# Optimization experiments

Hardware: AMD Instinct MI355X
Metric: run time of the kernel (lower is better)

## Reference

```python
import jax, jax.numpy as jnp
import numpy as np

B, S, D = 32, 1, 2048
H, KVH, HD = 16, 4, 128
MAXS = 4096
EPS = 1e-5
NREP = H // KVH  # GQA repeat factor = 4
FF = 4 * D
POS = 4095  # decode position (start_pos)


def setup_inputs() -> dict:
    key = jax.random.key(0)
    ks = jax.random.split(key, 12)
    sc = lambda d: 1.0 / np.sqrt(d)
    # RoPE angles for the current token position, [S, HD//2]
    inv_freq = 1.0 / (10000.0 ** (np.arange(0, HD, 2, dtype=np.float32) / HD))
    ang = (POS + np.arange(S, dtype=np.float32))[:, None] * inv_freq[None, :]
    return {
        "x": jax.random.normal(ks[0], (B, S, D), jnp.float32),
        "cos": jnp.asarray(np.cos(ang), jnp.float32),
        "sin": jnp.asarray(np.sin(ang), jnp.float32),
        "k_cache": jax.random.normal(ks[1], (B, MAXS, KVH, HD), jnp.float32),
        "v_cache": jax.random.normal(ks[2], (B, MAXS, KVH, HD), jnp.float32),
        "w_rms_attn": jnp.ones((D,), jnp.float32),
        "wq": jax.random.normal(ks[3], (D, D), jnp.float32) * sc(D),
        "wk": jax.random.normal(ks[4], (D, KVH * HD), jnp.float32) * sc(D),
        "wv": jax.random.normal(ks[5], (D, KVH * HD), jnp.float32) * sc(D),
        "wo": jax.random.normal(ks[6], (D, D), jnp.float32) * sc(D),
        "w_rms_ffn": jnp.ones((D,), jnp.float32),
        "w1": jax.random.normal(ks[7], (D, FF), jnp.float32) * sc(D),
        "w2": jax.random.normal(ks[8], (D, FF), jnp.float32) * sc(D),
        "w3": jax.random.normal(ks[9], (FF, D), jnp.float32) * sc(FF),
        "start_pos": POS,
    }


def _rmsnorm(x, g):
    return x * g * jax.lax.rsqrt(jnp.mean(x * x, axis=-1, keepdims=True) + EPS)


def _rope(x, cos, sin):
    # x: [B, S, h, HD]; complex rotation on (even, odd) pairs
    xr = x.reshape(*x.shape[:-1], HD // 2, 2)
    x0, x1 = xr[..., 0], xr[..., 1]
    c = cos[None, :, None, :]
    s = sin[None, :, None, :]
    r0 = x0 * c - x1 * s
    r1 = x0 * s + x1 * c
    return jnp.stack([r0, r1], axis=-1).reshape(x.shape)


def reference(x, cos, sin, k_cache, v_cache, w_rms_attn, wq, wk, wv, wo,
              w_rms_ffn, w1, w2, w3, start_pos):
    xa = _rmsnorm(x, w_rms_attn)
    xq = (xa @ wq).reshape(B, S, H, HD)
    xk = (xa @ wk).reshape(B, S, KVH, HD)
    xv = (xa @ wv).reshape(B, S, KVH, HD)
    # Source applies RoPE to K and V (not Q) -- reproduced faithfully.
    xk = _rope(xk, cos, sin)
    xv = _rope(xv, cos, sin)
    kc = jax.lax.dynamic_update_slice(k_cache, xk, (0, start_pos, 0, 0))
    vc = jax.lax.dynamic_update_slice(v_cache, xv, (0, start_pos, 0, 0))
    klen = start_pos + S
    keys = jnp.repeat(kc[:, :klen], NREP, axis=2)   # [B, klen, H, HD]
    vals = jnp.repeat(vc[:, :klen], NREP, axis=2)
    att = jnp.einsum('bqhd,bkhd->bhqk', xq, keys) * (HD ** -0.5)
    att = jax.nn.softmax(att, axis=-1)
    y = jnp.einsum('bhqk,bkhd->bqhd', att, vals).reshape(B, S, D)
    h = x + y @ wo
    xf = _rmsnorm(h, w_rms_ffn)
    return h + (jax.nn.silu(xf @ w1) * (xf @ w2)) @ w3
```

## Files before the change

### kernel.cpp

```cpp
#include <hip/hip_runtime.h>
#include <math.h>

#define BB 32
#define DD 2048
#define NKVH 4
#define HDIM 128
#define MAXS 4096
#define FFD 8192
#define POS 4095
#define EPSV 1e-5f
#define SCALE 0.08838834764831845f
#define ASPLIT 16

#define OFF_QT   0u
#define OFF_KT   65536u
#define OFF_VT   81920u
#define OFF_G1   98304u
#define OFF_G2   360448u
#define ZERO_N   622592u
#define OFF_XAT  622592u
#define OFF_RK   688128u
#define OFF_RV   704512u
#define OFF_PML  720896u
#define OFF_PACC 737280u
#define OFF_YT   1785856u
#define OFF_H    1851392u
#define OFF_XFT  1916928u

#define REP32(M) M(0) M(1) M(2) M(3) M(4) M(5) M(6) M(7) M(8) M(9) M(10) M(11) M(12) M(13) M(14) M(15) M(16) M(17) M(18) M(19) M(20) M(21) M(22) M(23) M(24) M(25) M(26) M(27) M(28) M(29) M(30) M(31)
#define REP32A(M,X) M(0,X) M(1,X) M(2,X) M(3,X) M(4,X) M(5,X) M(6,X) M(7,X) M(8,X) M(9,X) M(10,X) M(11,X) M(12,X) M(13,X) M(14,X) M(15,X) M(16,X) M(17,X) M(18,X) M(19,X) M(20,X) M(21,X) M(22,X) M(23,X) M(24,X) M(25,X) M(26,X) M(27,X) M(28,X) M(29,X) M(30,X) M(31,X)

#define DECLA(i) float a##i = 0.f;
#define FMA1(i,k) a##i = fmaf(ap[(k)*32 + (i)], w##k, a##i);
#define STORET(i) tl[i] = a##i;
#define ATOMN(i) atomicAdd(C + (size_t)(i)*N + n, a##i);

template<int N, int CH, bool TOUT>
__device__ __forceinline__ void gemv_body(const float* __restrict__ At,
                                          const float* __restrict__ W,
                                          float* __restrict__ C, int colblk,
                                          float* tile) {
    int tid = (int)threadIdx.x;
    int n = colblk * 256 + tid;
    int d0 = blockIdx.y * CH;
    const float* Wp = W + (size_t)d0 * N + n;
    const float* ap = At + (size_t)d0 * 32;
    REP32(DECLA)
#pragma unroll 4
    for (int dd = 0; dd < CH; dd += 4) {
        float w0 = Wp[0];
        float w1 = Wp[(size_t)N];
        float w2 = Wp[(size_t)N * 2];
        float w3 = Wp[(size_t)N * 3];
        REP32A(FMA1, 0)
        REP32A(FMA1, 1)
        REP32A(FMA1, 2)
        REP32A(FMA1, 3)
        Wp += (size_t)N * 4;
        ap += 128;
    }
    if constexpr (TOUT) {
        float* tl = tile + tid * 33;
        REP32(STORET)
        __syncthreads();
        float* cb = C + (size_t)colblk * 256 * 32;
#pragma unroll
        for (int i = 0; i < 32; ++i) {
            int f = i * 256 + tid;
            atomicAdd(cb + f, tile[(f >> 5) * 33 + (f & 31)]);
        }
    } else {
        REP32(ATOMN)
    }
}

template<int N, int CH, bool TOUT>
__global__ __launch_bounds__(256) void gemv32_kernel(const float* __restrict__ At,
                                                     const float* __restrict__ W,
                                                     float* __restrict__ C) {
    if constexpr (TOUT) {
        __shared__ float tile[256 * 33];
        gemv_body<N, CH, true>(At, W, C, blockIdx.x, tile);
    } else {
        gemv_body<N, CH, false>(At, W, C, blockIdx.x, nullptr);
    }
}

template<int N, int CH, int HALF>
__global__ __launch_bounds__(256) void gemv32_dual_kernel(const float* __restrict__ At,
        const float* __restrict__ W0, const float* __restrict__ W1,
        float* __restrict__ C0, float* __restrict__ C1) {
    __shared__ float tile[256 * 33];
    int bx = blockIdx.x;
    if (bx < HALF) gemv_body<N, CH, true>(At, W0, C0, bx, tile);
    else           gemv_body<N, CH, true>(At, W1, C1, bx - HALF, tile);
}

__global__ void zero_kernel(float* __restrict__ p) {
    p[blockIdx.x * 256 + threadIdx.x] = 0.f;
}

__global__ void rmsnorm_kernel(const float* __restrict__ in, const float* __restrict__ g,
                               float* __restrict__ outT, float* __restrict__ cpy) {
    int b = blockIdx.x;
    int tid = threadIdx.x;
    const float* row = in + b * DD;
    float v[8];
    float ss = 0.f;
#pragma unroll
    for (int i = 0; i < 8; ++i) { v[i] = row[tid + i * 256]; ss += v[i] * v[i]; }
#pragma unroll
    for (int off = 32; off; off >>= 1) ss += __shfl_xor(ss, off);
    __shared__ float red[4];
    if ((tid & 63) == 0) red[tid >> 6] = ss;
    __syncthreads();
    ss = red[0] + red[1] + red[2] + red[3];
    float scale = rsqrtf(ss * (1.f / DD) + EPSV);
#pragma unroll
    for (int i = 0; i < 8; ++i) {
        int idx = tid + i * 256;
        outT[(size_t)idx * 32 + b] = v[i] * g[idx] * scale;
        if (cpy) cpy[b * DD + idx] = v[i];
    }
}

__global__ void rope_kernel(const float* __restrict__ kT, const float* __restrict__ vT,
                            const float* __restrict__ cosb, const float* __restrict__ sinb,
                            float* __restrict__ rk, float* __restrict__ rv) {
    int idx = blockIdx.x * 256 + threadIdx.x;
    int b = idx >> 8, rem = idx & 255;
    int kvh = rem >> 6, i = rem & 63;
    float c = cosb[i], s = sinb[i];
    int col = kvh * HDIM + 2 * i;
    float k0 = kT[(size_t)col * 32 + b], k1 = kT[(size_t)(col + 1) * 32 + b];
    float v0 = vT[(size_t)col * 32 + b], v1 = vT[(size_t)(col + 1) * 32 + b];
    int o = (b * NKVH + kvh) * HDIM + 2 * i;
    rk[o] = k0 * c - k1 * s; rk[o + 1] = k0 * s + k1 * c;
    rv[o] = v0 * c - v1 * s; rv[o + 1] = v0 * s + v1 * c;
}

__global__ __launch_bounds__(256) void attn_partial_kernel(
    const float* __restrict__ qT, const float* __restrict__ kc, const float* __restrict__ vc,
    const float* __restrict__ rk, const float* __restrict__ rv,
    float* __restrict__ pml, float* __restrict__ pacc) {
    int bid = blockIdx.x;
    int split = bid & 15, kvh = (bid >> 4) & 3, b = bid >> 6;
    int tid = threadIdx.x;
    __shared__ float q_s[4][HDIM];
    __shared__ float p_s[4][256];
    __shared__ float red[8][4][HDIM];
    for (int i = tid; i < 4 * HDIM; i += 256)
        q_s[i >> 7][i & 127] = qT[(size_t)(kvh * 512 + i) * 32 + b];
    __syncthreads();
    int t0 = split * 256;
    {
        int t = t0 + tid;
        const float* krow = (t == POS) ? rk + (b * NKVH + kvh) * HDIM
                                       : kc + ((size_t)(b * MAXS + t) * NKVH + kvh) * HDIM;
        float s0 = 0, s1 = 0, s2 = 0, s3 = 0;
#pragma unroll 8
        for (int j = 0; j < HDIM; j += 4) {
            float4 kk = *(const float4*)(krow + j);
            s0 += kk.x * q_s[0][j] + kk.y * q_s[0][j + 1] + kk.z * q_s[0][j + 2] + kk.w * q_s[0][j + 3];
            s1 += kk.x * q_s[1][j] + kk.y * q_s[1][j + 1] + kk.z * q_s[1][j + 2] + kk.w * q_s[1][j + 3];
            s2 += kk.x * q_s[2][j] + kk.y * q_s[2][j + 1] + kk.z * q_s[2][j + 2] + kk.w * q_s[2][j + 3];
            s3 += kk.x * q_s[3][j] + kk.y * q_s[3][j + 1] + kk.z * q_s[3][j + 2] + kk.w * q_s[3][j + 3];
        }
        p_s[0][tid] = s0 * SCALE; p_s[1][tid] = s1 * SCALE;
        p_s[2][tid] = s2 * SCALE; p_s[3][tid] = s3 * SCALE;
    }
    __syncthreads();
    {
        int w = tid >> 6, lane = tid & 63;
        float e0 = p_s[w][lane], e1 = p_s[w][lane + 64];
        float e2 = p_s[w][lane + 128], e3 = p_s[w][lane + 192];
        float m = fmaxf(fmaxf(e0, e1), fmaxf(e2, e3));
#pragma unroll
        for (int off = 32; off; off >>= 1) m = fmaxf(m, __shfl_xor(m, off));
        e0 = __expf(e0 - m); e1 = __expf(e1 - m);
        e2 = __expf(e2 - m); e3 = __expf(e3 - m);
        p_s[w][lane] = e0; p_s[w][lane + 64] = e1;
        p_s[w][lane + 128] = e2; p_s[w][lane + 192] = e3;
        float l = e0 + e1 + e2 + e3;
#pragma unroll
        for (int off = 32; off; off >>= 1) l += __shfl_xor(l, off);
        if (lane == 0) {
            int idx = ((b * NKVH + kvh) * ASPLIT + split) * 4 + w;
            pml[2 * idx] = m; pml[2 * idx + 1] = l;
        }
    }
    __syncthreads();
    {
        int tsub = tid >> 5, q4 = tid & 31;
        int tb = t0 + tsub * 32;
        const float* vbase = vc + ((size_t)(b * MAXS + tb) * NKVH + kvh) * HDIM + q4 * 4;
        float4 a0 = {0, 0, 0, 0}, a1 = a0, a2 = a0, a3 = a0;
        int jmax = (split == ASPLIT - 1 && tsub == 7) ? 31 : 32;
#pragma unroll 4
        for (int j = 0; j < jmax; ++j) {
            float4 vv = *(const float4*)(vbase + (size_t)j * (NKVH * HDIM));
            int tl = tsub * 32 + j;
            float p0 = p_s[0][tl], p1 = p_s[1][tl], p2 = p_s[2][tl], p3 = p_s[3][tl];
            a0.x = fmaf(p0, vv.x, a0.x); a0.y = fmaf(p0, vv.y, a0.y); a0.z = fmaf(p0, vv.z, a0.z); a0.w = fmaf(p0, vv.w, a0.w);
            a1.x = fmaf(p1, vv.x, a1.x); a1.y = fmaf(p1, vv.y, a1.y); a1.z = fmaf(p1, vv.z, a1.z); a1.w = fmaf(p1, vv.w, a1.w);
            a2.x = fmaf(p2, vv.x, a2.x); a2.y = fmaf(p2, vv.y, a2.y); a2.z = fmaf(p2, vv.z, a2.z); a2.w = fmaf(p2, vv.w, a2.w);
            a3.x = fmaf(p3, vv.x, a3.x); a3.y = fmaf(p3, vv.y, a3.y); a3.z = fmaf(p3, vv.z, a3.z); a3.w = fmaf(p3, vv.w, a3.w);
        }
        if (split == ASPLIT - 1 && tsub == 7) {
            float4 vv = *(const float4*)(rv + (b * NKVH + kvh) * HDIM + q4 * 4);
            float p0 = p_s[0][255], p1 = p_s[1][255], p2 = p_s[2][255], p3 = p_s[3][255];
            a0.x = fmaf(p0, vv.x, a0.x); a0.y = fmaf(p0, vv.y, a0.y); a0.z = fmaf(p0, vv.z, a0.z); a0.w = fmaf(p0, vv.w, a0.w);
            a1.x = fmaf(p1, vv.x, a1.x); a1.y = fmaf(p1, vv.y, a1.y); a1.z = fmaf(p1, vv.z, a1.z); a1.w = fmaf(p1, vv.w, a1.w);
            a2.x = fmaf(p2, vv.x, a2.x); a2.y = fmaf(p2, vv.y, a2.y); a2.z = fmaf(p2, vv.z, a2.z); a2.w = fmaf(p2, vv.w, a2.w);
            a3.x = fmaf(p3, vv.x, a3.x); a3.y = fmaf(p3, vv.y, a3.y); a3.z = fmaf(p3, vv.z, a3.z); a3.w = fmaf(p3, vv.w, a3.w);
        }
        *(float4*)&red[tsub][0][q4 * 4] = a0;
        *(float4*)&red[tsub][1][q4 * 4] = a1;
        *(float4*)&red[tsub][2][q4 * 4] = a2;
        *(float4*)&red[tsub][3][q4 * 4] = a3;
    }
    __syncthreads();
    if (tid < 128) {
        int h = tid >> 5, qq = tid & 31;
        float4 s = {0, 0, 0, 0};
#pragma unroll
        for (int r = 0; r < 8; ++r) {
            float4 t4 = *(const float4*)&red[r][h][qq * 4];
            s.x += t4.x; s.y += t4.y; s.z += t4.z; s.w += t4.w;
        }
        int idx = ((b * NKVH + kvh) * ASPLIT + split) * 4 + h;
        *(float4*)(pacc + (size_t)idx * HDIM + qq * 4) = s;
    }
}

__global__ void attn_combine_kernel(const float* __restrict__ pml,
                                    const float* __restrict__ pacc, float* __restrict__ yT) {
    int bid = blockIdx.x;
    int b = bid >> 4, h = bid & 15;
    int kvh = h >> 2, hl = h & 3;
    int d = threadIdx.x;
    float M = -INFINITY;
#pragma unroll
    for (int s = 0; s < ASPLIT; ++s) {
        int idx = ((b * NKVH + kvh) * ASPLIT + s) * 4 + hl;
        M = fmaxf(M, pml[2 * idx]);
    }
    float denom = 0.f, acc = 0.f;
#pragma unroll
    for (int s = 0; s < ASPLIT; ++s) {
        int idx = ((b * NKVH + kvh) * ASPLIT + s) * 4 + hl;
        float e = __expf(pml[2 * idx] - M);
        denom += pml[2 * idx + 1] * e;
        acc += e * pacc[(size_t)idx * HDIM + d];
    }
    yT[(size_t)(h * HDIM + d) * 32 + b] = acc / denom;
}

__global__ void silu_mul_kernel(float* __restrict__ g1, const float* __restrict__ g2) {
    int i = blockIdx.x * 256 + threadIdx.x;
    float a = g1[i], bb = g2[i];
    g1[i] = a * bb / (1.f + __expf(-a));
}

extern "C" void kernel_launch(void* const* d_in, const int* in_sizes, int n_in,
                              void* d_out, int out_size, void* d_ws, size_t ws_size,
                              hipStream_t stream) {
    (void)in_sizes; (void)n_in; (void)out_size; (void)ws_size;
    const float* x    = (const float*)d_in[0];
    const float* cosb = (const float*)d_in[1];
    const float* sinb = (const float*)d_in[2];
    const float* kc   = (const float*)d_in[3];
    const float* vc   = (const float*)d_in[4];
    const float* wra  = (const float*)d_in[5];
    const float* wq   = (const float*)d_in[6];
    const float* wk   = (const float*)d_in[7];
    const float* wv   = (const float*)d_in[8];
    const float* wo   = (const float*)d_in[9];
    const float* wrf  = (const float*)d_in[10];
    const float* w1   = (const float*)d_in[11];
    const float* w2   = (const float*)d_in[12];
    const float* w3   = (const float*)d_in[13];
    float* out = (float*)d_out;
    float* ws  = (float*)d_ws;

    float* qT   = ws + OFF_QT;
    float* kT   = ws + OFF_KT;
    float* vT   = ws + OFF_VT;
    float* g1T  = ws + OFF_G1;
    float* g2T  = ws + OFF_G2;
    float* xaT  = ws + OFF_XAT;
    float* rk   = ws + OFF_RK;
    float* rv   = ws + OFF_RV;
    float* pml  = ws + OFF_PML;
    float* pacc = ws + OFF_PACC;
    float* yT   = ws + OFF_YT;
    float* h    = ws + OFF_H;
    float* xfT  = ws + OFF_XFT;

    zero_kernel<<<ZERO_N / 256, 256, 0, stream>>>(ws);

    rmsnorm_kernel<<<32, 256, 0, stream>>>(x, wra, xaT, h);
    gemv32_kernel<2048, 32, true><<<dim3(8, 64), 256, 0, stream>>>(xaT, wq, qT);
    gemv32_dual_kernel<512, 32, 2><<<dim3(4, 64), 256, 0, stream>>>(xaT, wk, wv, kT, vT);
    rope_kernel<<<32, 256, 0, stream>>>(kT, vT, cosb, sinb, rk, rv);
    attn_partial_kernel<<<2048, 256, 0, stream>>>(qT, kc, vc, rk, rv, pml, pacc);
    attn_combine_kernel<<<512, 128, 0, stream>>>(pml, pacc, yT);
    gemv32_kernel<2048, 32, false><<<dim3(8, 64), 256, 0, stream>>>(yT, wo, h);
    rmsnorm_kernel<<<32, 256, 0, stream>>>(h, wrf, xfT, out);
    gemv32_dual_kernel<8192, 128, 32><<<dim3(64, 16), 256, 0, stream>>>(xfT, w1, w2, g1T, g2T);
    silu_mul_kernel<<<1024, 256, 0, stream>>>(g1T, g2T);
    gemv32_kernel<2048, 128, false><<<dim3(8, 64), 256, 0, stream>>>(g1T, w3, out);
}
```

Baseline: 296.7 us.

## Pipeline attention loads, deepen GEMV unroll and chunking, fold RoPE into a fix buffer

The attention kernel's QK and PV loops are replaced by manually double-buffered register loads (two banks of eight float4 loads), so memory latency on the KV cache overlaps with the FMAs. The GEMV body now loads eight weight rows per iteration, and the Q/O/W3 GEMVs use larger per-block reduction chunks with fewer blocks, which halves the number of atomic partial sums. Q is written directly in row-major form instead of through the transposed shared-tile path. The RoPE kernel becomes a fix-up kernel that writes a 16-position tail copy of K/V, with the current token rotated; only one of those positions is actually read. The rework adds register pressure and some redundant copying in exchange for fewer atomics and better load overlap.

```diff
diff --git a/kernel.cpp b/kernel.cpp
--- a/kernel.cpp
+++ b/kernel.cpp
@@ -11,6 +11,7 @@
 #define EPSV 1e-5f
 #define SCALE 0.08838834764831845f
 #define ASPLIT 16
+#define SPOS 256
 
 #define OFF_QT   0u
 #define OFF_KT   65536u
@@ -19,13 +20,13 @@
 #define OFF_G2   360448u
 #define ZERO_N   622592u
 #define OFF_XAT  622592u
-#define OFF_RK   688128u
-#define OFF_RV   704512u
 #define OFF_PML  720896u
 #define OFF_PACC 737280u
 #define OFF_YT   1785856u
 #define OFF_H    1851392u
 #define OFF_XFT  1916928u
+#define OFF_KFIX 1982464u
+#define OFF_VFIX 2244608u
 
 #define REP32(M) M(0) M(1) M(2) M(3) M(4) M(5) M(6) M(7) M(8) M(9) M(10) M(11) M(12) M(13) M(14) M(15) M(16) M(17) M(18) M(19) M(20) M(21) M(22) M(23) M(24) M(25) M(26) M(27) M(28) M(29) M(30) M(31)
 #define REP32A(M,X) M(0,X) M(1,X) M(2,X) M(3,X) M(4,X) M(5,X) M(6,X) M(7,X) M(8,X) M(9,X) M(10,X) M(11,X) M(12,X) M(13,X) M(14,X) M(15,X) M(16,X) M(17,X) M(18,X) M(19,X) M(20,X) M(21,X) M(22,X) M(23,X) M(24,X) M(25,X) M(26,X) M(27,X) M(28,X) M(29,X) M(30,X) M(31,X)
@@ -34,6 +35,7 @@
 #define FMA1(i,k) a##i = fmaf(ap[(k)*32 + (i)], w##k, a##i);
 #define STORET(i) tl[i] = a##i;
 #define ATOMN(i) atomicAdd(C + (size_t)(i)*N + n, a##i);
+#define LDW(k) float w##k = Wp[(size_t)N * (k)];
 
 template<int N, int CH, bool TOUT>
 __device__ __forceinline__ void gemv_body(const float* __restrict__ At,
@@ -46,18 +48,19 @@
     const float* Wp = W + (size_t)d0 * N + n;
     const float* ap = At + (size_t)d0 * 32;
     REP32(DECLA)
-#pragma unroll 4
-    for (int dd = 0; dd < CH; dd += 4) {
-        float w0 = Wp[0];
-        float w1 = Wp[(size_t)N];
-        float w2 = Wp[(size_t)N * 2];
-        float w3 = Wp[(size_t)N * 3];
+#pragma unroll 2
+    for (int dd = 0; dd < CH; dd += 8) {
+        LDW(0) LDW(1) LDW(2) LDW(3) LDW(4) LDW(5) LDW(6) LDW(7)
         REP32A(FMA1, 0)
         REP32A(FMA1, 1)
         REP32A(FMA1, 2)
         REP32A(FMA1, 3)
-        Wp += (size_t)N * 4;
-        ap += 128;
+        REP32A(FMA1, 4)
+        REP32A(FMA1, 5)
+        REP32A(FMA1, 6)
+        REP32A(FMA1, 7)
+        Wp += (size_t)N * 8;
+        ap += 256;
     }
     if constexpr (TOUT) {
         float* tl = tile + tid * 33;
@@ -124,48 +127,104 @@
     }
 }
 
-__global__ void rope_kernel(const float* __restrict__ kT, const float* __restrict__ vT,
-                            const float* __restrict__ cosb, const float* __restrict__ sinb,
-                            float* __restrict__ rk, float* __restrict__ rv) {
+__global__ void fixrope_kernel(const float* __restrict__ kc, const float* __restrict__ vc,
+                               const float* __restrict__ kT, const float* __restrict__ vT,
+                               const float* __restrict__ cosb, const float* __restrict__ sinb,
+                               float* __restrict__ kfix, float* __restrict__ vfix) {
     int idx = blockIdx.x * 256 + threadIdx.x;
-    int b = idx >> 8, rem = idx & 255;
-    int kvh = rem >> 6, i = rem & 63;
-    float c = cosb[i], s = sinb[i];
-    int col = kvh * HDIM + 2 * i;
-    float k0 = kT[(size_t)col * 32 + b], k1 = kT[(size_t)(col + 1) * 32 + b];
-    float v0 = vT[(size_t)col * 32 + b], v1 = vT[(size_t)(col + 1) * 32 + b];
-    int o = (b * NKVH + kvh) * HDIM + 2 * i;
-    rk[o] = k0 * c - k1 * s; rk[o + 1] = k0 * s + k1 * c;
-    rv[o] = v0 * c - v1 * s; rv[o + 1] = v0 * s + v1 * c;
-}
-
-__global__ __launch_bounds__(256) void attn_partial_kernel(
-    const float* __restrict__ qT, const float* __restrict__ kc, const float* __restrict__ vc,
-    const float* __restrict__ rk, const float* __restrict__ rv,
+    int b = idx >> 13, rem = idx & 8191;
+    int pos = rem >> 9, col = rem & 511;
+    int gpos = 4080 + pos;
+    float kv, vv;
+    if (gpos == POS) {
+        int d = col & 127, i = d >> 1;
+        float c = cosb[i], s = sinb[i];
+        int colp = col & ~1;
+        float k0 = kT[(size_t)colp * 32 + b], k1 = kT[(size_t)(colp + 1) * 32 + b];
+        float v0 = vT[(size_t)colp * 32 + b], v1 = vT[(size_t)(colp + 1) * 32 + b];
+        if (d & 1) { kv = k0 * s + k1 * c; vv = v0 * s + v1 * c; }
+        else       { kv = k0 * c - k1 * s; vv = v0 * c - v1 * s; }
+    } else {
+        size_t o = ((size_t)(b * MAXS + gpos)) * 512 + col;
+        kv = kc[o]; vv = vc[o];
+    }
+    kfix[idx] = kv; vfix[idx] = vv;
+}
+
+
+#define QKSTEP(KK,D0) \
+    s0 = fmaf(KK.x, q_s[0][D0], s0); s0 = fmaf(KK.y, q_s[0][(D0)+1], s0); \
+    s0 = fmaf(KK.z, q_s[0][(D0)+2], s0); s0 = fmaf(KK.w, q_s[0][(D0)+3], s0); \
+    s1 = fmaf(KK.x, q_s[1][D0], s1); s1 = fmaf(KK.y, q_s[1][(D0)+1], s1); \
+    s1 = fmaf(KK.z, q_s[1][(D0)+2], s1); s1 = fmaf(KK.w, q_s[1][(D0)+3], s1); \
+    s2 = fmaf(KK.x, q_s[2][D0], s2); s2 = fmaf(KK.y, q_s[2][(D0)+1], s2); \
+    s2 = fmaf(KK.z, q_s[2][(D0)+2], s2); s2 = fmaf(KK.w, q_s[2][(D0)+3], s2); \
+    s3 = fmaf(KK.x, q_s[3][D0], s3); s3 = fmaf(KK.y, q_s[3][(D0)+1], s3); \
+    s3 = fmaf(KK.z, q_s[3][(D0)+2], s3); s3 = fmaf(KK.w, q_s[3][(D0)+3], s3);
+
+#define QKLOAD(S,JB) \
+    S##0 = *(const float4*)(krow + (JB)*32 + 0);  S##1 = *(const float4*)(krow + (JB)*32 + 4); \
+    S##2 = *(const float4*)(krow + (JB)*32 + 8);  S##3 = *(const float4*)(krow + (JB)*32 + 12); \
+    S##4 = *(const float4*)(krow + (JB)*32 + 16); S##5 = *(const float4*)(krow + (JB)*32 + 20); \
+    S##6 = *(const float4*)(krow + (JB)*32 + 24); S##7 = *(const float4*)(krow + (JB)*32 + 28);
+
+#define QKFMA(S,JB) \
+    QKSTEP(S##0,(JB)*32+0)  QKSTEP(S##1,(JB)*32+4)  QKSTEP(S##2,(JB)*32+8)  QKSTEP(S##3,(JB)*32+12) \
+    QKSTEP(S##4,(JB)*32+16) QKSTEP(S##5,(JB)*32+20) QKSTEP(S##6,(JB)*32+24) QKSTEP(S##7,(JB)*32+28)
+
+#define PVSTEP(VV,P0,P1,P2,P3) \
+    a0.x = fmaf(P0, VV.x, a0.x); a0.y = fmaf(P0, VV.y, a0.y); a0.z = fmaf(P0, VV.z, a0.z); a0.w = fmaf(P0, VV.w, a0.w); \
+    a1.x = fmaf(P1, VV.x, a1.x); a1.y = fmaf(P1, VV.y, a1.y); a1.z = fmaf(P1, VV.z, a1.z); a1.w = fmaf(P1, VV.w, a1.w); \
+    a2.x = fmaf(P2, VV.x, a2.x); a2.y = fmaf(P2, VV.y, a2.y); a2.z = fmaf(P2, VV.z, a2.z); a2.w = fmaf(P2, VV.w, a2.w); \
+    a3.x = fmaf(P3, VV.x, a3.x); a3.y = fmaf(P3, VV.y, a3.y); a3.z = fmaf(P3, VV.z, a3.z); a3.w = fmaf(P3, VV.w, a3.w);
+
+#define PVLOAD(S,JB) \
+    S##0 = *(const float4*)(vbase + (size_t)((JB)*8+0)*512); S##1 = *(const float4*)(vbase + (size_t)((JB)*8+1)*512); \
+    S##2 = *(const float4*)(vbase + (size_t)((JB)*8+2)*512); S##3 = *(const float4*)(vbase + (size_t)((JB)*8+3)*512); \
+    S##4 = *(const float4*)(vbase + (size_t)((JB)*8+4)*512); S##5 = *(const float4*)(vbase + (size_t)((JB)*8+5)*512); \
+    S##6 = *(const float4*)(vbase + (size_t)((JB)*8+6)*512); S##7 = *(const float4*)(vbase + (size_t)((JB)*8+7)*512);
+
+#define PVFMA(S,JB) { \
+    int tl = tsub * 32 + (JB) * 8; \
+    float4 pa0 = *(const float4*)&p_s[0][tl], pb0 = *(const float4*)&p_s[0][tl + 4]; \
+    float4 pa1 = *(const float4*)&p_s[1][tl], pb1 = *(const float4*)&p_s[1][tl + 4]; \
+    float4 pa2 = *(const float4*)&p_s[2][tl], pb2 = *(const float4*)&p_s[2][tl + 4]; \
+    float4 pa3 = *(const float4*)&p_s[3][tl], pb3 = *(const float4*)&p_s[3][tl + 4]; \
+    PVSTEP(S##0, pa0.x, pa1.x, pa2.x, pa3.x) \
+    PVSTEP(S##1, pa0.y, pa1.y, pa2.y, pa3.y) \
+    PVSTEP(S##2, pa0.z, pa1.z, pa2.z, pa3.z) \
+    PVSTEP(S##3, pa0.w, pa1.w, pa2.w, pa3.w) \
+    PVSTEP(S##4, pb0.x, pb1.x, pb2.x, pb3.x) \
+    PVSTEP(S##5, pb0.y, pb1.y, pb2.y, pb3.y) \
+    PVSTEP(S##6, pb0.z, pb1.z, pb2.z, pb3.z) \
+    PVSTEP(S##7, pb0.w, pb1.w, pb2.w, pb3.w) }
+
+__global__ __launch_bounds__(256) void attn_mlp_kernel(
+    const float* __restrict__ qn, const float* __restrict__ kc, const float* __restrict__ vc,
+    const float* __restrict__ kfix, const float* __restrict__ vfix,
     float* __restrict__ pml, float* __restrict__ pacc) {
     int bid = blockIdx.x;
     int split = bid & 15, kvh = (bid >> 4) & 3, b = bid >> 6;
     int tid = threadIdx.x;
     __shared__ float q_s[4][HDIM];
-    __shared__ float p_s[4][256];
+    __shared__ float p_s[4][SPOS];
     __shared__ float red[8][4][HDIM];
-    for (int i = tid; i < 4 * HDIM; i += 256)
-        q_s[i >> 7][i & 127] = qT[(size_t)(kvh * 512 + i) * 32 + b];
-    __syncthreads();
-    int t0 = split * 256;
+    for (int i = tid; i < 512; i += 256)
+        q_s[i >> 7][i & 127] = qn[(size_t)b * DD + kvh * 512 + i];
+    __syncthreads();
+    int t0 = split * SPOS;
     {
         int t = t0 + tid;
-        const float* krow = (t == POS) ? rk + (b * NKVH + kvh) * HDIM
-                                       : kc + ((size_t)(b * MAXS + t) * NKVH + kvh) * HDIM;
-        float s0 = 0, s1 = 0, s2 = 0, s3 = 0;
-#pragma unroll 8
-        for (int j = 0; j < HDIM; j += 4) {
-            float4 kk = *(const float4*)(krow + j);
-            s0 += kk.x * q_s[0][j] + kk.y * q_s[0][j + 1] + kk.z * q_s[0][j + 2] + kk.w * q_s[0][j + 3];
-            s1 += kk.x * q_s[1][j] + kk.y * q_s[1][j + 1] + kk.z * q_s[1][j + 2] + kk.w * q_s[1][j + 3];
-            s2 += kk.x * q_s[2][j] + kk.y * q_s[2][j + 1] + kk.z * q_s[2][j + 2] + kk.w * q_s[2][j + 3];
-            s3 += kk.x * q_s[3][j] + kk.y * q_s[3][j + 1] + kk.z * q_s[3][j + 2] + kk.w * q_s[3][j + 3];
-        }
+        const float* krow = (t == POS)
+            ? kfix + (size_t)b * 8192 + 15 * 512 + kvh * HDIM
+            : kc + ((size_t)(b * MAXS + t) * NKVH + kvh) * HDIM;
+        float s0 = 0.f, s1 = 0.f, s2 = 0.f, s3 = 0.f;
+        float4 A0, A1, A2, A3, A4, A5, A6, A7, B0, B1, B2, B3, B4, B5, B6, B7;
+        QKLOAD(A, 0)
+        QKLOAD(B, 1) QKFMA(A, 0)
+        QKLOAD(A, 2) QKFMA(B, 1)
+        QKLOAD(B, 3) QKFMA(A, 2)
+        QKFMA(B, 3)
         p_s[0][tid] = s0 * SCALE; p_s[1][tid] = s1 * SCALE;
         p_s[2][tid] = s2 * SCALE; p_s[3][tid] = s3 * SCALE;
     }
@@ -192,28 +251,18 @@
     __syncthreads();
     {
         int tsub = tid >> 5, q4 = tid & 31;
-        int tb = t0 + tsub * 32;
-        const float* vbase = vc + ((size_t)(b * MAXS + tb) * NKVH + kvh) * HDIM + q4 * 4;
+        const float* vbase = vc + ((size_t)(b * MAXS + t0 + tsub * 32) * NKVH + kvh) * HDIM + q4 * 4;
+        bool lastt = (split == ASPLIT - 1 && tsub == 7);
         float4 a0 = {0, 0, 0, 0}, a1 = a0, a2 = a0, a3 = a0;
-        int jmax = (split == ASPLIT - 1 && tsub == 7) ? 31 : 32;
-#pragma unroll 4
-        for (int j = 0; j < jmax; ++j) {
-            float4 vv = *(const float4*)(vbase + (size_t)j * (NKVH * HDIM));
-            int tl = tsub * 32 + j;
-            float p0 = p_s[0][tl], p1 = p_s[1][tl], p2 = p_s[2][tl], p3 = p_s[3][tl];
-            a0.x = fmaf(p0, vv.x, a0.x); a0.y = fmaf(p0, vv.y, a0.y); a0.z = fmaf(p0, vv.z, a0.z); a0.w = fmaf(p0, vv.w, a0.w);
-            a1.x = fmaf(p1, vv.x, a1.x); a1.y = fmaf(p1, vv.y, a1.y); a1.z = fmaf(p1, vv.z, a1.z); a1.w = fmaf(p1, vv.w, a1.w);
-            a2.x = fmaf(p2, vv.x, a2.x); a2.y = fmaf(p2, vv.y, a2.y); a2.z = fmaf(p2, vv.z, a2.z); a2.w = fmaf(p2, vv.w, a2.w);
-            a3.x = fmaf(p3, vv.x, a3.x); a3.y = fmaf(p3, vv.y, a3.y); a3.z = fmaf(p3, vv.z, a3.z); a3.w = fmaf(p3, vv.w, a3.w);
-        }
-        if (split == ASPLIT - 1 && tsub == 7) {
-            float4 vv = *(const float4*)(rv + (b * NKVH + kvh) * HDIM + q4 * 4);
-            float p0 = p_s[0][255], p1 = p_s[1][255], p2 = p_s[2][255], p3 = p_s[3][255];
-            a0.x = fmaf(p0, vv.x, a0.x); a0.y = fmaf(p0, vv.y, a0.y); a0.z = fmaf(p0, vv.z, a0.z); a0.w = fmaf(p0, vv.w, a0.w);
-            a1.x = fmaf(p1, vv.x, a1.x); a1.y = fmaf(p1, vv.y, a1.y); a1.z = fmaf(p1, vv.z, a1.z); a1.w = fmaf(p1, vv.w, a1.w);
-            a2.x = fmaf(p2, vv.x, a2.x); a2.y = fmaf(p2, vv.y, a2.y); a2.z = fmaf(p2, vv.z, a2.z); a2.w = fmaf(p2, vv.w, a2.w);
-            a3.x = fmaf(p3, vv.x, a3.x); a3.y = fmaf(p3, vv.y, a3.y); a3.z = fmaf(p3, vv.z, a3.z); a3.w = fmaf(p3, vv.w, a3.w);
-        }
+        float4 A0, A1, A2, A3, A4, A5, A6, A7, B0, B1, B2, B3, B4, B5, B6, B7;
+        PVLOAD(A, 0)
+        PVLOAD(B, 1) PVFMA(A, 0)
+        PVLOAD(A, 2) PVFMA(B, 1)
+        PVLOAD(B, 3)
+        if (lastt)
+            B7 = *(const float4*)(vfix + (size_t)b * 8192 + 15 * 512 + kvh * HDIM + q4 * 4);
+        PVFMA(A, 2)
+        PVFMA(B, 3)
         *(float4*)&red[tsub][0][q4 * 4] = a0;
         *(float4*)&red[tsub][1][q4 * 4] = a1;
         *(float4*)&red[tsub][2][q4 * 4] = a2;
@@ -240,13 +289,11 @@
     int kvh = h >> 2, hl = h & 3;
     int d = threadIdx.x;
     float M = -INFINITY;
-#pragma unroll
-    for (int s = 0; s < ASPLIT; ++s) {
-        int idx = ((b * NKVH + kvh) * ASPLIT + s) * 4 + hl;
-        M = fmaxf(M, pml[2 * idx]);
-    }
+#pragma unroll 8
+    for (int s = 0; s < ASPLIT; ++s)
+        M = fmaxf(M, pml[(((b * NKVH + kvh) * ASPLIT + s) * 4 + hl) * 2]);
     float denom = 0.f, acc = 0.f;
-#pragma unroll
+#pragma unroll 4
     for (int s = 0; s < ASPLIT; ++s) {
         int idx = ((b * NKVH + kvh) * ASPLIT + s) * 4 + hl;
         float e = __expf(pml[2 * idx] - M);
@@ -283,31 +330,31 @@
     float* out = (float*)d_out;
     float* ws  = (float*)d_ws;
 
-    float* qT   = ws + OFF_QT;
+    float* qn   = ws + OFF_QT;
     float* kT   = ws + OFF_KT;
     float* vT   = ws + OFF_VT;
     float* g1T  = ws + OFF_G1;
     float* g2T  = ws + OFF_G2;
     float* xaT  = ws + OFF_XAT;
-    float* rk   = ws + OFF_RK;
-    float* rv   = ws + OFF_RV;
     float* pml  = ws + OFF_PML;
     float* pacc = ws + OFF_PACC;
     float* yT   = ws + OFF_YT;
     float* h    = ws + OFF_H;
     float* xfT  = ws + OFF_XFT;
+    float* kfix = ws + OFF_KFIX;
+    float* vfix = ws + OFF_VFIX;
 
     zero_kernel<<<ZERO_N / 256, 256, 0, stream>>>(ws);
 
     rmsnorm_kernel<<<32, 256, 0, stream>>>(x, wra, xaT, h);
-    gemv32_kernel<2048, 32, true><<<dim3(8, 64), 256, 0, stream>>>(xaT, wq, qT);
-    gemv32_dual_kernel<512, 32, 2><<<dim3(4, 64), 256, 0, stream>>>(xaT, wk, wv, kT, vT);
-    rope_kernel<<<32, 256, 0, stream>>>(kT, vT, cosb, sinb, rk, rv);
-    attn_partial_kernel<<<2048, 256, 0, stream>>>(qT, kc, vc, rk, rv, pml, pacc);
+    gemv32_kernel<2048, 64, false><<<dim3(8, 32), 256, 0, stream>>>(xaT, wq, qn);
+    gemv32_dual_kernel<512, 64, 2><<<dim3(4, 32), 256, 0, stream>>>(xaT, wk, wv, kT, vT);
+    fixrope_kernel<<<1024, 256, 0, stream>>>(kc, vc, kT, vT, cosb, sinb, kfix, vfix);
+    attn_mlp_kernel<<<2048, 256, 0, stream>>>(qn, kc, vc, kfix, vfix, pml, pacc);
     attn_combine_kernel<<<512, 128, 0, stream>>>(pml, pacc, yT);
-    gemv32_kernel<2048, 32, false><<<dim3(8, 64), 256, 0, stream>>>(yT, wo, h);
+    gemv32_kernel<2048, 64, false><<<dim3(8, 32), 256, 0, stream>>>(yT, wo, h);
     rmsnorm_kernel<<<32, 256, 0, stream>>>(h, wrf, xfT, out);
     gemv32_dual_kernel<8192, 128, 32><<<dim3(64, 16), 256, 0, stream>>>(xfT, w1, w2, g1T, g2T);
     silu_mul_kernel<<<1024, 256, 0, stream>>>(g1T, g2T);
-    gemv32_kernel<2048, 128, false><<<dim3(8, 64), 256, 0, stream>>>(g1T, w3, out);
-}
+    gemv32_kernel<2048, 256, false><<<dim3(8, 32), 256, 0, stream>>>(g1T, w3, out);
+}
```

After: 332.1 us. 11.9% more time.
